# Performance work log

Hardware: AMD Instinct MI355X
Metric: run time of the kernel (lower is better)

Reference implementation:

```python
import jax, jax.numpy as jnp
import numpy as np

EPS = 1e-06

def rotate_half(x):
    d = x.shape[-1] // 2
    return jnp.concatenate([-x[..., d:], x[..., :d]], axis=-1)

def rmsnorm(x, w):
    rms = jnp.sqrt(jnp.mean(x * x, axis=-1, keepdims=True) + EPS)
    return (x / rms) * w

def setup_inputs() -> dict:
    key = jax.random.key(0)
    ks = jax.random.split(key, 12)
    H, Hq, Hkv, Dh, S, C = 2048, 16, 8, 128, 1, 16384
    sc = 0.02
    return {
        "hidden_states": jax.random.normal(ks[0], (1, 1, S, H), jnp.float32),
        "cos": jax.random.uniform(ks[1], (1, 1, S, Dh), jnp.float32),
        "sin": jax.random.uniform(ks[2], (1, 1, S, Dh), jnp.float32),
        "attention_mask": jnp.zeros((1, 1, S, C + S), jnp.float32),
        "k_cache": jax.random.normal(ks[3], (Hkv, Dh, C), jnp.float32),
        "v_cache": jax.random.normal(ks[4], (Hkv, C, Dh), jnp.float32),
        "Wq": jax.random.normal(ks[5], (Hq, Dh, H), jnp.float32) * sc,
        "Wk": jax.random.normal(ks[6], (Hkv, Dh, H), jnp.float32) * sc,
        "Wv": jax.random.normal(ks[7], (Hkv, Dh, H), jnp.float32) * sc,
        "Wo": jax.random.normal(ks[8], (H, Hq * Dh), jnp.float32) * sc,
        "q_norm_w": jnp.ones((Dh,), jnp.float32),
        "k_norm_w": jnp.ones((Dh,), jnp.float32),
    }

def reference(hidden_states, cos, sin, attention_mask, k_cache, v_cache, Wq, Wk, Wv, Wo, q_norm_w, k_norm_w):
    S = hidden_states.shape[2]
    Hq, Dh = Wq.shape[0], Wq.shape[1]
    Hkv = Wk.shape[0]
    g = Hq // Hkv
    x = hidden_states.reshape(S, -1)                      # [S, H]
    # per-head 1x1 conv == per-head linear; batched as einsum
    q = rmsnorm(jnp.einsum('sh,qdh->qsd', x, Wq), q_norm_w)   # [Hq, S, Dh]
    k = rmsnorm(jnp.einsum('sh,kdh->ksd', x, Wk), k_norm_w)   # [Hkv, S, Dh]
    v = jnp.einsum('sh,kdh->ksd', x, Wv)                      # [Hkv, S, Dh]
    c = cos.reshape(S, Dh)
    s = sin.reshape(S, Dh)
    q = q * c + rotate_half(q) * s
    k_new = k * c + rotate_half(k) * s
    # KV cache concat: k stored transposed [Hkv, Dh, C]
    k_full = jnp.concatenate([k_cache, jnp.swapaxes(k_new, 1, 2)], axis=2)  # [Hkv, Dh, C+S]
    v_full = jnp.concatenate([v_cache, v], axis=1)                          # [Hkv, C+S, Dh]
    kf = jnp.repeat(k_full, g, axis=0)                    # GQA expand -> [Hq, Dh, C+S]
    vf = jnp.repeat(v_full, g, axis=0)                    # [Hq, C+S, Dh]
    scaling = Dh ** -0.5
    scores = jnp.einsum('qsd,qdc->qsc', q, kf) * scaling + attention_mask.reshape(1, S, -1)
    probs = jax.nn.softmax(scores, axis=-1)
    out = jnp.einsum('qsc,qcd->qsd', probs, vf)           # [Hq, S, Dh]
    out = jnp.transpose(out, (1, 0, 2)).reshape(S, Hq * Dh)  # head-major last dim
    attn = out @ Wo.T                                     # o_proj 1x1 conv
    return attn.reshape(1, 1, S, -1), k_new, v
```

## Files before the change

kernel.cpp:

```cpp
#include <hip/hip_runtime.h>
#include <math.h>
#include <stddef.h>

#define HQ   16
#define HKV  8
#define DH   128
#define HID  2048
#define CC   16384
#define SPAD 16896
#define NSCH 33
#define NAV  65


__global__ void k_qkv(const float* __restrict__ x,
                      const float* __restrict__ Wq,
                      const float* __restrict__ Wk,
                      const float* __restrict__ Wv,
                      float* __restrict__ raw){
  int wave = threadIdx.x >> 6, lane = threadIdx.x & 63;
  int e = blockIdx.x * 4 + wave;
  const float* W;
  if (e < 2048)      W = Wq + (size_t)e * HID;
  else if (e < 3072) W = Wk + (size_t)(e - 2048) * HID;
  else               W = Wv + (size_t)(e - 3072) * HID;
  float acc = 0.f;
  #pragma unroll
  for (int j = 0; j < 4; ++j){
    int base = (j * 64 + lane) * 8;
    float4 a0 = *(const float4*)(x + base);
    float4 a1 = *(const float4*)(x + base + 4);
    float4 b0 = *(const float4*)(W + base);
    float4 b1 = *(const float4*)(W + base + 4);
    acc += a0.x*b0.x + a0.y*b0.y + a0.z*b0.z + a0.w*b0.w
         + a1.x*b1.x + a1.y*b1.y + a1.z*b1.z + a1.w*b1.w;
  }
  #pragma unroll
  for (int off = 32; off; off >>= 1) acc += __shfl_down(acc, off, 64);
  if (lane == 0) raw[e] = acc;
}

__global__ void k_normrope(const float* __restrict__ raw,
                           const float* __restrict__ cosb,
                           const float* __restrict__ sinb,
                           const float* __restrict__ qw,
                           const float* __restrict__ kw,
                           float* __restrict__ qf,
                           float* __restrict__ kf,
                           float* __restrict__ out){
  __shared__ float lds[DH];
  __shared__ float wsum[2];
  int b = blockIdx.x, t = threadIdx.x;
  if (b >= 24){
    int h = b - 24;
    out[3072 + h * DH + t] = raw[3072 + h * DH + t];
    return;
  }
  bool isq = (b < 16);
  int h = isq ? b : b - 16;
  float val = isq ? raw[h * DH + t] : raw[2048 + h * DH + t];
  float ss = val * val;
  #pragma unroll
  for (int off = 32; off; off >>= 1) ss += __shfl_down(ss, off, 64);
  if ((t & 63) == 0) wsum[t >> 6] = ss;
  __syncthreads();
  float rms = sqrtf((wsum[0] + wsum[1]) / 128.f + 1e-6f);
  float w = isq ? qw[t] : kw[t];
  float normed = val / rms * w;
  lds[t] = normed;
  __syncthreads();
  float rot = (t < 64) ? -lds[t + 64] : lds[t - 64];
  float res = normed * cosb[t] + rot * sinb[t];
  if (isq) qf[h * DH + t] = res;
  else { kf[h * DH + t] = res; out[2048 + h * DH + t] = res; }
}

__global__ void k_scores(const float* __restrict__ qf,
                         const float* __restrict__ kf,
                         const float* __restrict__ kcache,
                         const float* __restrict__ mask,
                         float* __restrict__ S,
                         float* __restrict__ spart){
  __shared__ float q_s[2][DH];
  __shared__ float red[8];
  int kv = blockIdx.x / NSCH, ch = blockIdx.x % NSCH;
  int c0 = ch * 512;
  int t = threadIdx.x;
  q_s[t >> 7][t & 127] = qf[(kv * 2 + (t >> 7)) * DH + (t & 127)];
  __syncthreads();
  const float scale = 0.08838834764831845f;

  float sc[2][2];
  int cA = c0 + 2 * t;
  {
    float d0a = 0.f, d0b = 0.f, d1a = 0.f, d1b = 0.f;
    if (cA < CC){
      const float* kp = kcache + (size_t)kv * DH * CC + cA;
      #pragma unroll 8
      for (int d = 0; d < DH; ++d){
        float2 kk = *(const float2*)(kp + (size_t)d * CC);
        float q0 = q_s[0][d], q1 = q_s[1][d];
        d0a += q0 * kk.x; d0b += q0 * kk.y;
        d1a += q1 * kk.x; d1b += q1 * kk.y;
      }
      float mA = mask[cA], mB = mask[cA + 1];
      sc[0][0] = d0a * scale + mA; sc[0][1] = d0b * scale + mB;
      sc[1][0] = d1a * scale + mA; sc[1][1] = d1b * scale + mB;
      *(float2*)(S + (size_t)(kv * 2)     * SPAD + cA) = make_float2(sc[0][0], sc[0][1]);
      *(float2*)(S + (size_t)(kv * 2 + 1) * SPAD + cA) = make_float2(sc[1][0], sc[1][1]);
    } else if (cA == CC){
      const float* kp = kf + kv * DH;
      #pragma unroll 8
      for (int d = 0; d < DH; ++d){
        float kd = kp[d];
        d0a += q_s[0][d] * kd; d1a += q_s[1][d] * kd;
      }
      float mA = mask[cA];
      sc[0][0] = d0a * scale + mA; sc[1][0] = d1a * scale + mA;
      sc[0][1] = -1e30f; sc[1][1] = -1e30f;
      S[(size_t)(kv * 2)     * SPAD + cA] = sc[0][0];
      S[(size_t)(kv * 2 + 1) * SPAD + cA] = sc[1][0];
    } else {
      sc[0][0] = sc[0][1] = sc[1][0] = sc[1][1] = -1e30f;
    }
  }

  int wv = t >> 6, ln = t & 63;
  float lmax0 = fmaxf(sc[0][0], sc[0][1]);
  float lmax1 = fmaxf(sc[1][0], sc[1][1]);
  #pragma unroll
  for (int off = 32; off; off >>= 1){
    lmax0 = fmaxf(lmax0, __shfl_down(lmax0, off, 64));
    lmax1 = fmaxf(lmax1, __shfl_down(lmax1, off, 64));
  }
  if (ln == 0){ red[wv] = lmax0; red[4 + wv] = lmax1; }
  __syncthreads();
  float m0 = fmaxf(fmaxf(red[0], red[1]), fmaxf(red[2], red[3]));
  float m1 = fmaxf(fmaxf(red[4], red[5]), fmaxf(red[6], red[7]));
  float ls0 = __expf(sc[0][0] - m0) + __expf(sc[0][1] - m0);
  float ls1 = __expf(sc[1][0] - m1) + __expf(sc[1][1] - m1);
  #pragma unroll
  for (int off = 32; off; off >>= 1){
    ls0 += __shfl_down(ls0, off, 64);
    ls1 += __shfl_down(ls1, off, 64);
  }
  __syncthreads();
  if (ln == 0){ red[wv] = ls0; red[4 + wv] = ls1; }
  __syncthreads();
  if (t == 0){
    float l0 = red[0] + red[1] + red[2] + red[3];
    float l1 = red[4] + red[5] + red[6] + red[7];
    spart[((size_t)(kv * 2)     * NSCH + ch) * 2]     = m0;
    spart[((size_t)(kv * 2)     * NSCH + ch) * 2 + 1] = l0;
    spart[((size_t)(kv * 2 + 1) * NSCH + ch) * 2]     = m1;
    spart[((size_t)(kv * 2 + 1) * NSCH + ch) * 2 + 1] = l1;
  }
}

__global__ void k_red(const float* __restrict__ spart, float2* __restrict__ ML){
  int qh = blockIdx.x, lane = threadIdx.x;
  float m = -1e30f, l = 0.f;
  if (lane < NSCH){
    m = spart[((size_t)qh * NSCH + lane) * 2];
    l = spart[((size_t)qh * NSCH + lane) * 2 + 1];
  }
  float M = m;
  #pragma unroll
  for (int off = 32; off; off >>= 1) M = fmaxf(M, __shfl_down(M, off, 64));
  M = __shfl(M, 0, 64);
  float term = l * __expf(m - M);
  #pragma unroll
  for (int off = 32; off; off >>= 1) term += __shfl_down(term, off, 64);
  if (lane == 0) ML[qh] = make_float2(M, term);
}

__global__ void k_av(const float* __restrict__ S,
                     const float2* __restrict__ ML,
                     const float* __restrict__ vcache,
                     const float* __restrict__ vnew,
                     float* __restrict__ opart){
  __shared__ float part[2][8][DH];
  int kv = blockIdx.x / NAV, ch = blockIdx.x % NAV;
  int c0 = ch * 256;
  int t = threadIdx.x;
  int s = t >> 5, d4 = (t & 31) * 4;
  float2 ml0 = ML[kv * 2], ml1 = ML[kv * 2 + 1];
  float M0 = ml0.x, Li0 = 1.f / ml0.y;
  float M1 = ml1.x, Li1 = 1.f / ml1.y;
  const float* S0 = S + (size_t)(kv * 2)     * SPAD;
  const float* S1 = S + (size_t)(kv * 2 + 1) * SPAD;
  float4 a0 = make_float4(0.f, 0.f, 0.f, 0.f);
  float4 a1 = make_float4(0.f, 0.f, 0.f, 0.f);
  for (int i = 0; i < 32; ++i){
    int c = c0 + i * 8 + s;
    if (c > CC) break;
    float p0 = __expf(S0[c] - M0);
    float p1 = __expf(S1[c] - M1);
    float4 v = (c < CC) ? *(const float4*)(vcache + ((size_t)kv * CC + c) * DH + d4)
                        : *(const float4*)(vnew + kv * DH + d4);
    a0.x += p0 * v.x; a0.y += p0 * v.y; a0.z += p0 * v.z; a0.w += p0 * v.w;
    a1.x += p1 * v.x; a1.y += p1 * v.y; a1.z += p1 * v.z; a1.w += p1 * v.w;
  }
  *(float4*)&part[0][s][d4] = a0;
  *(float4*)&part[1][s][d4] = a1;
  __syncthreads();
  {
    int hh = t >> 7, d = t & 127;
    float o = 0.f;
    #pragma unroll
    for (int ss = 0; ss < 8; ++ss) o += part[hh][ss][d];
    float Li = hh ? Li1 : Li0;
    int qh = kv * 2 + hh;
    opart[((size_t)qh * NAV + ch) * DH + d] = o * Li;
  }
}

__global__ void k_osum(const float* __restrict__ opart, float* __restrict__ attn_in){
  int qh = blockIdx.x, d = threadIdx.x;
  float o = 0.f;
  for (int ch = 0; ch < NAV; ++ch)
    o += opart[((size_t)qh * NAV + ch) * DH + d];
  attn_in[qh * DH + d] = o;
}

__global__ void k_oproj(const float* __restrict__ attn_in,
                        const float* __restrict__ Wo,
                        float* __restrict__ out){
  int wave = threadIdx.x >> 6, lane = threadIdx.x & 63;
  int e = blockIdx.x * 4 + wave;
  const float* W = Wo + (size_t)e * HID;
  float acc = 0.f;
  #pragma unroll
  for (int j = 0; j < 4; ++j){
    int base = (j * 64 + lane) * 8;
    float4 a0 = *(const float4*)(attn_in + base);
    float4 a1 = *(const float4*)(attn_in + base + 4);
    float4 b0 = *(const float4*)(W + base);
    float4 b1 = *(const float4*)(W + base + 4);
    acc += a0.x*b0.x + a0.y*b0.y + a0.z*b0.z + a0.w*b0.w
         + a1.x*b1.x + a1.y*b1.y + a1.z*b1.z + a1.w*b1.w;
  }
  #pragma unroll
  for (int off = 32; off; off >>= 1) acc += __shfl_down(acc, off, 64);
  if (lane == 0) out[e] = acc;
}

extern "C" void kernel_launch(void* const* d_in, const int* in_sizes, int n_in,
                              void* d_out, int out_size, void* d_ws, size_t ws_size,
                              hipStream_t stream){
  const float* x    = (const float*)d_in[0];
  const float* cosb = (const float*)d_in[1];
  const float* sinb = (const float*)d_in[2];
  const float* mask = (const float*)d_in[3];
  const float* kc   = (const float*)d_in[4];
  const float* vc   = (const float*)d_in[5];
  const float* Wq   = (const float*)d_in[6];
  const float* Wk   = (const float*)d_in[7];
  const float* Wv   = (const float*)d_in[8];
  const float* Wo   = (const float*)d_in[9];
  const float* qw   = (const float*)d_in[10];
  const float* kw   = (const float*)d_in[11];
  float* out = (float*)d_out;
  float* ws = (float*)d_ws;
  float* raw     = ws;
  float* qf      = ws + 4096;
  float* kf      = ws + 6144;
  float* S       = ws + 8192;
  float* spart   = ws + 278528;
  float2* ML     = (float2*)(ws + 279584);
  float* opart   = ws + 279616;
  float* attn_in = ws + 412736;

  k_qkv     <<<1024, 256, 0, stream>>>(x, Wq, Wk, Wv, raw);
  k_normrope<<<32,   128, 0, stream>>>(raw, cosb, sinb, qw, kw, qf, kf, out);
  k_scores  <<<HKV * NSCH, 256, 0, stream>>>(qf, kf, kc, mask, S, spart);
  k_red     <<<HQ, 64, 0, stream>>>(spart, ML);
  k_av      <<<HKV * NAV, 256, 0, stream>>>(S, ML, vc, raw + 3072, opart);
  k_osum    <<<HQ, DH, 0, stream>>>(opart, attn_in);
  k_oproj   <<<512, 256, 0, stream>>>(attn_in, Wo, out);
}
```

Before: 240.8 us.

## Halve score chunk size and move new-token AV term into osum

The scores kernel now handles one key per thread (256 keys per block, 65 chunks), which doubles the block count for more parallelism over the K-cache read but gives up the float2 loads. The AV kernel drops the extra 65th chunk that held only the new token. That token's contribution is added in k_osum, which removes the branch and early break from the AV loop, and the loop is unrolled. k_red now does an online max/sum merge so it can take more than 64 partials.

```diff
diff --git a/kernel.cpp b/kernel.cpp
--- a/kernel.cpp
+++ b/kernel.cpp
@@ -8,8 +8,8 @@
 #define HID  2048
 #define CC   16384
 #define SPAD 16896
-#define NSCH 33
-#define NAV  65
+#define NSCH 65
+#define NAV  64
 
 
 __global__ void k_qkv(const float* __restrict__ x,
@@ -83,50 +83,48 @@
   __shared__ float q_s[2][DH];
   __shared__ float red[8];
   int kv = blockIdx.x / NSCH, ch = blockIdx.x % NSCH;
-  int c0 = ch * 512;
+  int c0 = ch * 256;
   int t = threadIdx.x;
   q_s[t >> 7][t & 127] = qf[(kv * 2 + (t >> 7)) * DH + (t & 127)];
   __syncthreads();
   const float scale = 0.08838834764831845f;
 
-  float sc[2][2];
-  int cA = c0 + 2 * t;
-  {
-    float d0a = 0.f, d0b = 0.f, d1a = 0.f, d1b = 0.f;
-    if (cA < CC){
-      const float* kp = kcache + (size_t)kv * DH * CC + cA;
-      #pragma unroll 8
-      for (int d = 0; d < DH; ++d){
-        float2 kk = *(const float2*)(kp + (size_t)d * CC);
-        float q0 = q_s[0][d], q1 = q_s[1][d];
-        d0a += q0 * kk.x; d0b += q0 * kk.y;
-        d1a += q1 * kk.x; d1b += q1 * kk.y;
-      }
-      float mA = mask[cA], mB = mask[cA + 1];
-      sc[0][0] = d0a * scale + mA; sc[0][1] = d0b * scale + mB;
-      sc[1][0] = d1a * scale + mA; sc[1][1] = d1b * scale + mB;
-      *(float2*)(S + (size_t)(kv * 2)     * SPAD + cA) = make_float2(sc[0][0], sc[0][1]);
-      *(float2*)(S + (size_t)(kv * 2 + 1) * SPAD + cA) = make_float2(sc[1][0], sc[1][1]);
-    } else if (cA == CC){
-      const float* kp = kf + kv * DH;
-      #pragma unroll 8
-      for (int d = 0; d < DH; ++d){
-        float kd = kp[d];
-        d0a += q_s[0][d] * kd; d1a += q_s[1][d] * kd;
-      }
-      float mA = mask[cA];
-      sc[0][0] = d0a * scale + mA; sc[1][0] = d1a * scale + mA;
-      sc[0][1] = -1e30f; sc[1][1] = -1e30f;
-      S[(size_t)(kv * 2)     * SPAD + cA] = sc[0][0];
-      S[(size_t)(kv * 2 + 1) * SPAD + cA] = sc[1][0];
-    } else {
-      sc[0][0] = sc[0][1] = sc[1][0] = sc[1][1] = -1e30f;
+  int c = c0 + t;
+  float s0, s1;
+  if (c < CC){
+    const float* kp = kcache + (size_t)kv * DH * CC + c;
+    float a0 = 0.f, a1 = 0.f;
+    #pragma unroll 8
+    for (int d = 0; d < DH; ++d){
+      float kd = kp[(size_t)d * CC];
+      a0 += q_s[0][d] * kd;
+      a1 += q_s[1][d] * kd;
     }
+    float mk = mask[c];
+    s0 = a0 * scale + mk;
+    s1 = a1 * scale + mk;
+    S[(size_t)(kv * 2)     * SPAD + c] = s0;
+    S[(size_t)(kv * 2 + 1) * SPAD + c] = s1;
+  } else if (c == CC){
+    const float* kp = kf + kv * DH;
+    float a0 = 0.f, a1 = 0.f;
+    #pragma unroll 8
+    for (int d = 0; d < DH; ++d){
+      float kd = kp[d];
+      a0 += q_s[0][d] * kd;
+      a1 += q_s[1][d] * kd;
+    }
+    float mk = mask[c];
+    s0 = a0 * scale + mk;
+    s1 = a1 * scale + mk;
+    S[(size_t)(kv * 2)     * SPAD + c] = s0;
+    S[(size_t)(kv * 2 + 1) * SPAD + c] = s1;
+  } else {
+    s0 = -1e30f; s1 = -1e30f;
   }
 
   int wv = t >> 6, ln = t & 63;
-  float lmax0 = fmaxf(sc[0][0], sc[0][1]);
-  float lmax1 = fmaxf(sc[1][0], sc[1][1]);
+  float lmax0 = s0, lmax1 = s1;
   #pragma unroll
   for (int off = 32; off; off >>= 1){
     lmax0 = fmaxf(lmax0, __shfl_down(lmax0, off, 64));
@@ -136,8 +134,8 @@
   __syncthreads();
   float m0 = fmaxf(fmaxf(red[0], red[1]), fmaxf(red[2], red[3]));
   float m1 = fmaxf(fmaxf(red[4], red[5]), fmaxf(red[6], red[7]));
-  float ls0 = __expf(sc[0][0] - m0) + __expf(sc[0][1] - m0);
-  float ls1 = __expf(sc[1][0] - m1) + __expf(sc[1][1] - m1);
+  float ls0 = __expf(s0 - m0);
+  float ls1 = __expf(s1 - m1);
   #pragma unroll
   for (int off = 32; off; off >>= 1){
     ls0 += __shfl_down(ls0, off, 64);
@@ -158,29 +156,32 @@
 
 __global__ void k_red(const float* __restrict__ spart, float2* __restrict__ ML){
   int qh = blockIdx.x, lane = threadIdx.x;
-  float m = -1e30f, l = 0.f;
-  if (lane < NSCH){
-    m = spart[((size_t)qh * NSCH + lane) * 2];
-    l = spart[((size_t)qh * NSCH + lane) * 2 + 1];
-  }
-  float M = m;
-  #pragma unroll
-  for (int off = 32; off; off >>= 1) M = fmaxf(M, __shfl_down(M, off, 64));
-  M = __shfl(M, 0, 64);
-  float term = l * __expf(m - M);
-  #pragma unroll
-  for (int off = 32; off; off >>= 1) term += __shfl_down(term, off, 64);
-  if (lane == 0) ML[qh] = make_float2(M, term);
+  float M = -1e30f, L = 0.f;
+  for (int j = lane; j < NSCH; j += 64){
+    float mj = spart[((size_t)qh * NSCH + j) * 2];
+    float lj = spart[((size_t)qh * NSCH + j) * 2 + 1];
+    float nM = fmaxf(M, mj);
+    L = L * __expf(M - nM) + lj * __expf(mj - nM);
+    M = nM;
+  }
+  #pragma unroll
+  for (int off = 32; off; off >>= 1){
+    float Mo = __shfl_down(M, off, 64);
+    float Lo = __shfl_down(L, off, 64);
+    float nM = fmaxf(M, Mo);
+    L = L * __expf(M - nM) + Lo * __expf(Mo - nM);
+    M = nM;
+  }
+  if (lane == 0) ML[qh] = make_float2(M, L);
 }
 
 __global__ void k_av(const float* __restrict__ S,
                      const float2* __restrict__ ML,
                      const float* __restrict__ vcache,
-                     const float* __restrict__ vnew,
                      float* __restrict__ opart){
   __shared__ float part[2][8][DH];
-  int kv = blockIdx.x / NAV, ch = blockIdx.x % NAV;
-  int c0 = ch * 256;
+  int kv = blockIdx.x >> 6, ch = blockIdx.x & 63;
+  int c0 = ch << 8;
   int t = threadIdx.x;
   int s = t >> 5, d4 = (t & 31) * 4;
   float2 ml0 = ML[kv * 2], ml1 = ML[kv * 2 + 1];
@@ -188,15 +189,15 @@
   float M1 = ml1.x, Li1 = 1.f / ml1.y;
   const float* S0 = S + (size_t)(kv * 2)     * SPAD;
   const float* S1 = S + (size_t)(kv * 2 + 1) * SPAD;
+  const float* vbase = vcache + (size_t)kv * CC * DH + d4;
   float4 a0 = make_float4(0.f, 0.f, 0.f, 0.f);
   float4 a1 = make_float4(0.f, 0.f, 0.f, 0.f);
+  #pragma unroll 4
   for (int i = 0; i < 32; ++i){
     int c = c0 + i * 8 + s;
-    if (c > CC) break;
     float p0 = __expf(S0[c] - M0);
     float p1 = __expf(S1[c] - M1);
-    float4 v = (c < CC) ? *(const float4*)(vcache + ((size_t)kv * CC + c) * DH + d4)
-                        : *(const float4*)(vnew + kv * DH + d4);
+    float4 v = *(const float4*)(vbase + (size_t)c * DH);
     a0.x += p0 * v.x; a0.y += p0 * v.y; a0.z += p0 * v.z; a0.w += p0 * v.w;
     a1.x += p1 * v.x; a1.y += p1 * v.y; a1.z += p1 * v.z; a1.w += p1 * v.w;
   }
@@ -214,11 +215,19 @@
   }
 }
 
-__global__ void k_osum(const float* __restrict__ opart, float* __restrict__ attn_in){
+__global__ void k_osum(const float* __restrict__ opart,
+                       const float* __restrict__ S,
+                       const float2* __restrict__ ML,
+                       const float* __restrict__ vnew,
+                       float* __restrict__ attn_in){
   int qh = blockIdx.x, d = threadIdx.x;
+  int kv = qh >> 1;
   float o = 0.f;
   for (int ch = 0; ch < NAV; ++ch)
     o += opart[((size_t)qh * NAV + ch) * DH + d];
+  float2 ml = ML[qh];
+  float pn = __expf(S[(size_t)qh * SPAD + CC] - ml.x) / ml.y;
+  o += pn * vnew[kv * DH + d];
   attn_in[qh * DH + d] = o;
 }
 
@@ -266,15 +275,15 @@
   float* kf      = ws + 6144;
   float* S       = ws + 8192;
   float* spart   = ws + 278528;
-  float2* ML     = (float2*)(ws + 279584);
-  float* opart   = ws + 279616;
-  float* attn_in = ws + 412736;
+  float2* ML     = (float2*)(ws + 280608);
+  float* opart   = ws + 280640;
+  float* attn_in = ws + 411712;
 
   k_qkv     <<<1024, 256, 0, stream>>>(x, Wq, Wk, Wv, raw);
   k_normrope<<<32,   128, 0, stream>>>(raw, cosb, sinb, qw, kw, qf, kf, out);
   k_scores  <<<HKV * NSCH, 256, 0, stream>>>(qf, kf, kc, mask, S, spart);
   k_red     <<<HQ, 64, 0, stream>>>(spart, ML);
-  k_av      <<<HKV * NAV, 256, 0, stream>>>(S, ML, vc, raw + 3072, opart);
-  k_osum    <<<HQ, DH, 0, stream>>>(opart, attn_in);
+  k_av      <<<HKV * NAV, 256, 0, stream>>>(S, ML, vc, opart);
+  k_osum    <<<HQ, DH, 0, stream>>>(opart, S, ML, raw + 3072, attn_in);
   k_oproj   <<<512, 256, 0, stream>>>(attn_in, Wo, out);
 }
```

After: 217.8 us. -9.6%, faster.
